# Kernel optimization log

Measured on AMD Instinct MI355X. Metric: run time of the kernel, lower is better.

The kernel has to match this reference:

```python
import jax, jax.numpy as jnp
import numpy as np

B, C, W, H = 4, 256, 64, 64
CQ = C // 8


def setup_inputs() -> dict:
    key = jax.random.key(0)
    ks = jax.random.split(key, 8)
    s = 1.0 / np.sqrt(C)
    return {
        "x": jax.random.normal(ks[0], (B, C, W, H), dtype=jnp.float32),
        "Wq": jax.random.normal(ks[1], (CQ, C), dtype=jnp.float32) * s,
        "bq": jnp.zeros((CQ,), dtype=jnp.float32),
        "Wk": jax.random.normal(ks[2], (CQ, C), dtype=jnp.float32) * s,
        "bk": jnp.zeros((CQ,), dtype=jnp.float32),
        "Wv": jax.random.normal(ks[3], (C, C), dtype=jnp.float32) * s,
        "bv": jnp.zeros((C,), dtype=jnp.float32),
        "gamma": jnp.zeros((1,), dtype=jnp.float32),
    }


def reference(x, Wq, bq, Wk, bk, Wv, bv, gamma):
    b, c, w, h = x.shape
    n = w * h
    xf = x.reshape(b, c, n)  # [B, C, N] flattened spatial
    # 1x1 convs are channel-wise linear maps
    q = jnp.einsum("dc,bcn->bnd", Wq, xf) + bq  # [B, N, C//8]
    k = jnp.einsum("dc,bcn->bdn", Wk, xf) + bk[None, :, None]  # [B, C//8, N]
    v = jnp.einsum("dc,bcn->bdn", Wv, xf) + bv[None, :, None]  # [B, C, N]
    attn = jax.nn.softmax(jnp.einsum("bnd,bdm->bnm", q, k), axis=-1)  # [B, N, N]
    # out[b, c, n] = sum_m v[b, c, m] * attn[b, n, m]
    out = jnp.einsum("bdm,bnm->bdn", v, attn).reshape(b, c, w, h)
    return gamma[0] * out + x
```

## Files before the change

kernel.cpp:

```cpp
#include <hip/hip_runtime.h>
#include <hip/hip_bf16.h>

#define CC 256
#define NN 4096
#define CQ 32
#define LOG2E 1.4426950408889634f

using short4v = __attribute__((ext_vector_type(4))) short;
using short8 = __attribute__((ext_vector_type(8))) short;
using f32x4  = __attribute__((ext_vector_type(4))) float;

static __device__ __forceinline__ short f2bf(float f) {
  __hip_bfloat16 h = __float2bfloat16(f);
  return *reinterpret_cast<short*>(&h);
}

__global__ __launch_bounds__(256) void prep_kernel(
    const float* __restrict__ Wq, const float* __restrict__ Wk,
    const float* __restrict__ Wv, __hip_bfloat16* __restrict__ Wf)
{
  int t = blockIdx.x*256 + threadIdx.x;
  int lane = t & 63, frag = t >> 6;
  int tile = frag >> 3, kc = frag & 7;
  int l15 = lane & 15, quad = lane >> 4;
  int R = tile*16 + l15;
  int k0 = kc*32 + quad*8;
  const float* src;
  if (R < 32)       src = Wq + (size_t)R*CC + k0;
  else if (R < 64)  src = Wk + (size_t)(R-32)*CC + k0;
  else              src = Wv + (size_t)(R-64)*CC + k0;
  float4 a = *(const float4*)(src);
  float4 c = *(const float4*)(src + 4);
  short8 o;
  o[0]=f2bf(a.x); o[1]=f2bf(a.y); o[2]=f2bf(a.z); o[3]=f2bf(a.w);
  o[4]=f2bf(c.x); o[5]=f2bf(c.y); o[6]=f2bf(c.z); o[7]=f2bf(c.w);
  *reinterpret_cast<short8*>(reinterpret_cast<short*>(Wf) + (size_t)t*8) = o;
}

__global__ __launch_bounds__(512, 4) void qkv_kernel(
    const float* __restrict__ x, const __hip_bfloat16* __restrict__ Wf,
    const float* __restrict__ bq, const float* __restrict__ bk,
    const float* __restrict__ bv,
    __hip_bfloat16* __restrict__ qb, __hip_bfloat16* __restrict__ kb,
    __hip_bfloat16* __restrict__ vb)
{
  const int b  = blockIdx.y;
  const int n0 = blockIdx.x * 32;
  const int tid = threadIdx.x;
  const int lane = tid & 63;
  const int w = __builtin_amdgcn_readfirstlane(tid >> 6);
  const int l15 = lane & 15, quad = lane >> 4;

  __shared__ __align__(16) short Xl[16*64*8];
  __shared__ __align__(16) short Vr[8][16][32];

  const float* xb = x + (size_t)b*CC*NN;
#pragma unroll
  for (int i = 0; i < 2; i++) {
    int s = tid + 512*i;
    int g = s >> 6, ln = s & 63;
    int nr = g >> 3, kc = g & 7;
    int l15s = ln & 15, quads = ln >> 4;
    int n = n0 + nr*16 + l15s;
    int c0 = kc*32 + quads*8;
    float v[8];
#pragma unroll
    for (int j = 0; j < 8; j++) v[j] = xb[(size_t)(c0 + j)*NN + n];
    short8 sv;
#pragma unroll
    for (int j = 0; j < 8; j++) sv[j] = f2bf(v[j]);
    *reinterpret_cast<short8*>(&Xl[(size_t)s*8]) = sv;
  }
  __syncthreads();

  const short* wfp = reinterpret_cast<const short*>(Wf);
  short* qb_s = reinterpret_cast<short*>(qb) + (size_t)b*NN*CQ;
  short* kb_s = reinterpret_cast<short*>(kb) + (size_t)b*NN*CQ;
  short* vb_s = reinterpret_cast<short*>(vb) + (size_t)b*CC*NN;

#define QKV_TILE(T) { \
    const int t_ = (T); \
    short8 Af[8]; \
    _Pragma("unroll") \
    for (int kc = 0; kc < 8; kc++) \
      Af[kc] = *(const short8*)(wfp + ((size_t)(t_*8 + kc)*64 + lane)*8); \
    f32x4 ac0 = {0.f,0.f,0.f,0.f}, ac1 = {0.f,0.f,0.f,0.f}; \
    _Pragma("unroll") \
    for (int kc = 0; kc < 8; kc++) { \
      short8 B0 = *(const short8*)(&Xl[((     kc)*64 + lane)*8]); \
      short8 B1 = *(const short8*)(&Xl[((8 +  kc)*64 + lane)*8]); \
      ac0 = __builtin_amdgcn_mfma_f32_16x16x32_bf16(Af[kc], B0, ac0, 0,0,0); \
      ac1 = __builtin_amdgcn_mfma_f32_16x16x32_bf16(Af[kc], B1, ac1, 0,0,0); \
    } \
    if (t_ < 2) { \
      int d0 = t_*16 + quad*4; \
      short4v p0, p1; \
      _Pragma("unroll") \
      for (int r = 0; r < 4; r++) { \
        float bb = bq[d0 + r]; \
        p0[r] = f2bf(LOG2E*(ac0[r] + bb)); \
        p1[r] = f2bf(LOG2E*(ac1[r] + bb)); \
      } \
      *(short4v*)(qb_s + (size_t)(n0      + l15)*CQ + d0) = p0; \
      *(short4v*)(qb_s + (size_t)(n0 + 16 + l15)*CQ + d0) = p1; \
    } else if (t_ < 4) { \
      int d0 = (t_-2)*16 + quad*4; \
      short4v p0, p1; \
      _Pragma("unroll") \
      for (int r = 0; r < 4; r++) { \
        float bb = bk[d0 + r]; \
        p0[r] = f2bf(ac0[r] + bb); \
        p1[r] = f2bf(ac1[r] + bb); \
      } \
      *(short4v*)(kb_s + (size_t)(n0      + l15)*CQ + d0) = p0; \
      *(short4v*)(kb_s + (size_t)(n0 + 16 + l15)*CQ + d0) = p1; \
    } else { \
      int rv0 = (t_-4)*16; \
      _Pragma("unroll") \
      for (int r = 0; r < 4; r++) { \
        float bb = bv[rv0 + quad*4 + r]; \
        Vr[w][quad*4 + r][     l15] = f2bf(ac0[r] + bb); \
        Vr[w][quad*4 + r][16 + l15] = f2bf(ac1[r] + bb); \
      } \
      int row = lane >> 2, cb = (lane & 3)*8; \
      short8 tv = *(const short8*)(&Vr[w][row][cb]); \
      *(short8*)(vb_s + (size_t)(rv0 + row)*NN + n0 + cb) = tv; \
    } }

  QKV_TILE(w);
  QKV_TILE(8 + w);
  if (w < 4) { QKV_TILE(16 + w); }
#undef QKV_TILE
}

__global__ __launch_bounds__(1024, 4) void attn_kernel(
    const __hip_bfloat16* __restrict__ qb, const __hip_bfloat16* __restrict__ kb,
    const __hip_bfloat16* __restrict__ vb,
    const float* __restrict__ x, const float* __restrict__ gamma,
    float* __restrict__ out)
{
  const int Bk = blockIdx.x;
  const int b = (Bk & 7) >> 1;
  const int n0 = ((Bk >> 3)*2 + (Bk & 1)) * 64;
  const int tid = threadIdx.x;
  const int lane = tid & 63;
  const int w = __builtin_amdgcn_readfirstlane(tid >> 6);
  const int sg = w & 3;
  const int mh = (w >> 2) & 1;
  const int ph = w >> 3;
  const int l15 = lane & 15, quad = lane >> 4;
  const int mbase = mh*32 + ph*16;

  __shared__ __align__(16) short Vs[256][76];
  __shared__ __align__(16) short Ps[64][76];
  __shared__ float Lbuf[4][64];

  const short* qbase = (const short*)qb + (size_t)b*NN*CQ;
  const short* kbase = (const short*)kb + (size_t)b*NN*CQ;
  const short* vbase = (const short*)vb + (size_t)b*CC*NN;

  short8 aq = *(const short8*)(qbase + (size_t)(n0 + sg*16 + l15)*CQ + quad*8);

  const int vr = tid >> 2, sh = tid & 3;

  short* pdst = &Ps[sg*16 + l15][mbase + quad*4];

  short8 vfa, vfb, kf;
  vfa = *(const short8*)(vbase + (size_t)vr*NN + sh*16);
  vfb = *(const short8*)(vbase + (size_t)vr*NN + sh*16 + 8);
  kf  = *(const short8*)(kbase + (size_t)(mbase + l15)*CQ + quad*8);
  *(short8*)(&Vs[vr][sh*16    ]) = vfa;
  *(short8*)(&Vs[vr][sh*16 + 8]) = vfb;

  f32x4 acc[4][2];
#pragma unroll
  for (int cg = 0; cg < 4; cg++)
#pragma unroll
    for (int ng = 0; ng < 2; ng++) acc[cg][ng] = (f32x4){0.f,0.f,0.f,0.f};
  float lsum = 0.f;

  __syncthreads();

  for (int T = 0; T < 64; T++) {
    short8 nva, nvb, nk;
    if (T < 63) {
      const short* vp = vbase + (size_t)vr*NN + (T+1)*64 + sh*16;
      nva = *(const short8*)(vp);
      nvb = *(const short8*)(vp + 8);
      nk  = *(const short8*)(kbase + (size_t)((T+1)*64 + mbase + l15)*CQ + quad*8);
    }

    f32x4 z = {0.f,0.f,0.f,0.f};
    f32x4 S = __builtin_amdgcn_mfma_f32_16x16x32_bf16(kf, aq, z, 0,0,0);
    {
      short4v pk;
#pragma unroll
      for (int r = 0; r < 4; r++) {
        float e = __builtin_amdgcn_exp2f(S[r]);
        lsum += e;
        pk[r] = f2bf(e);
      }
      *(short4v*)(pdst) = pk;
    }
    __syncthreads();

    short8 ap0 = *(const short8*)(&Ps[(ph*2    )*16 + l15][mh*32 + quad*8]);
    short8 ap1 = *(const short8*)(&Ps[(ph*2 + 1)*16 + l15][mh*32 + quad*8]);
#pragma unroll
    for (int cg = 0; cg < 4; cg++) {
      short8 av = *(const short8*)(&Vs[sg*64 + cg*16 + l15][mh*32 + quad*8]);
      acc[cg][0] = __builtin_amdgcn_mfma_f32_16x16x32_bf16(av, ap0, acc[cg][0], 0,0,0);
      acc[cg][1] = __builtin_amdgcn_mfma_f32_16x16x32_bf16(av, ap1, acc[cg][1], 0,0,0);
    }
    __syncthreads();

    if (T < 63) {
      *(short8*)(&Vs[vr][sh*16    ]) = nva;
      *(short8*)(&Vs[vr][sh*16 + 8]) = nvb;
      kf = nk;
    }
  }

  {
    float s = lsum;
    s += __shfl_xor(s, 16); s += __shfl_xor(s, 32);
    if (quad == 0) Lbuf[mh*2 + ph][sg*16 + l15] = s;
  }

  float* poolf = reinterpret_cast<float*>(&Vs[0][0]);
  __syncthreads();
#pragma unroll
  for (int g = 0; g < 2; g++) {
    if (mh == 1 && (sg >> 1) == g) {
#pragma unroll
      for (int cg = 0; cg < 4; cg++)
#pragma unroll
        for (int ng = 0; ng < 2; ng++)
#pragma unroll
          for (int r = 0; r < 4; r++)
            poolf[(sg & 1)*4096 + (cg*16 + quad*4 + r)*64 + (ph*2 + ng)*16 + l15] = acc[cg][ng][r];
    }
    __syncthreads();
    if (mh == 0 && (sg >> 1) == g) {
#pragma unroll
      for (int cg = 0; cg < 4; cg++)
#pragma unroll
        for (int ng = 0; ng < 2; ng++)
#pragma unroll
          for (int r = 0; r < 4; r++)
            acc[cg][ng][r] += poolf[(sg & 1)*4096 + (cg*16 + quad*4 + r)*64 + (ph*2 + ng)*16 + l15];
    }
    __syncthreads();
  }

  if (mh == 0) {
    const float gm = gamma[0];
    float Lv[2];
#pragma unroll
    for (int ng = 0; ng < 2; ng++) {
      int n = (ph*2 + ng)*16 + l15;
      Lv[ng] = 1.0f / (Lbuf[0][n] + Lbuf[1][n] + Lbuf[2][n] + Lbuf[3][n]);
    }
#pragma unroll
    for (int cg = 0; cg < 4; cg++) {
#pragma unroll
      for (int ng = 0; ng < 2; ng++) {
#pragma unroll
        for (int r = 0; r < 4; r++) {
          size_t idx = ((size_t)b*CC + sg*64 + cg*16 + quad*4 + r)*NN + n0 + (ph*2 + ng)*16 + l15;
          out[idx] = gm * acc[cg][ng][r] * Lv[ng] + x[idx];
        }
      }
    }
  }
}

extern "C" void kernel_launch(void* const* d_in, const int* in_sizes, int n_in,
                              void* d_out, int out_size, void* d_ws, size_t ws_size,
                              hipStream_t stream) {
  const float* x     = (const float*)d_in[0];
  const float* Wq    = (const float*)d_in[1];
  const float* bq    = (const float*)d_in[2];
  const float* Wk    = (const float*)d_in[3];
  const float* bk    = (const float*)d_in[4];
  const float* Wv    = (const float*)d_in[5];
  const float* bv    = (const float*)d_in[6];
  const float* gamma = (const float*)d_in[7];
  float* out = (float*)d_out;

  char* ws = (char*)d_ws;
  if (ws_size < (11u << 20)) return;
  __hip_bfloat16* qb = (__hip_bfloat16*)(ws);
  __hip_bfloat16* kb = (__hip_bfloat16*)(ws + (1u << 20));
  __hip_bfloat16* vb = (__hip_bfloat16*)(ws + (2u << 20));
  __hip_bfloat16* Wf = (__hip_bfloat16*)(ws + (10u << 20));

  prep_kernel<<<dim3(40), 256, 0, stream>>>(Wq, Wk, Wv, Wf);
  qkv_kernel<<<dim3(128, 4), 512, 0, stream>>>(x, Wf, bq, bk, bv, qb, kb, vb);
  attn_kernel<<<dim3(256), 1024, 0, stream>>>(qb, kb, vb, x, gamma, out);
}
```

Measured before the change: 145.9 us.

## Fuse prep, QKV projection and attention into one cooperative kernel with grid syncs

Replaces three separate kernel launches with one cooperative kernel of 256 blocks that runs weight conversion, QKV projection and attention in sequence, separated by grid-wide syncs. Each block handles the same batch and position tile across phases and shares one static shared-memory buffer. The aim is to remove launch overhead and the gaps between kernels. In exchange it depends on cooperative launch succeeding with all 256 blocks of 1024 threads co-resident, and it adds grid.sync costs. If the cooperative launch fails it falls back to the old three launches.

```diff
diff --git a/kernel.cpp b/kernel.cpp
--- a/kernel.cpp
+++ b/kernel.cpp
@@ -1,5 +1,8 @@
 #include <hip/hip_runtime.h>
 #include <hip/hip_bf16.h>
+#include <hip/hip_cooperative_groups.h>
+
+namespace cg = cooperative_groups;
 
 #define CC 256
 #define NN 4096
@@ -13,6 +16,276 @@
 static __device__ __forceinline__ short f2bf(float f) {
   __hip_bfloat16 h = __float2bfloat16(f);
   return *reinterpret_cast<short*>(&h);
+}
+
+__global__ __launch_bounds__(1024, 4) void fused_kernel(
+    const float* __restrict__ x,
+    const float* __restrict__ Wq, const float* __restrict__ Wk,
+    const float* __restrict__ Wv,
+    const float* __restrict__ bq, const float* __restrict__ bk,
+    const float* __restrict__ bv,
+    const float* __restrict__ gamma,
+    __hip_bfloat16* __restrict__ Wf,
+    __hip_bfloat16* __restrict__ qb, __hip_bfloat16* __restrict__ kb,
+    __hip_bfloat16* __restrict__ vb,
+    float* __restrict__ out)
+{
+  cg::grid_group grid = cg::this_grid();
+  const int Bk = blockIdx.x;
+  const int tid = threadIdx.x;
+
+  __shared__ __align__(16) char smem[49664];
+
+  {
+    int t = Bk*1024 + tid;
+    if (t < 10240) {
+      int lane = t & 63, frag = t >> 6;
+      int tile = frag >> 3, kc = frag & 7;
+      int l15 = lane & 15, quad = lane >> 4;
+      int R = tile*16 + l15;
+      int k0 = kc*32 + quad*8;
+      const float* src;
+      if (R < 32)       src = Wq + (size_t)R*CC + k0;
+      else if (R < 64)  src = Wk + (size_t)(R-32)*CC + k0;
+      else              src = Wv + (size_t)(R-64)*CC + k0;
+      float4 a = *(const float4*)(src);
+      float4 c = *(const float4*)(src + 4);
+      short8 o;
+      o[0]=f2bf(a.x); o[1]=f2bf(a.y); o[2]=f2bf(a.z); o[3]=f2bf(a.w);
+      o[4]=f2bf(c.x); o[5]=f2bf(c.y); o[6]=f2bf(c.z); o[7]=f2bf(c.w);
+      *reinterpret_cast<short8*>(reinterpret_cast<short*>(Wf) + (size_t)t*8) = o;
+    }
+  }
+  grid.sync();
+
+  {
+    const int b    = (Bk & 7) >> 1;
+    const int half = tid >> 9;
+    const int n0   = ((Bk >> 3)*2 + (Bk & 1))*64 + half*32;
+    const int tid_h = tid & 511;
+    const int lane = tid & 63;
+    const int w  = tid_h >> 6;
+    const int w2 = tid >> 6;
+    const int l15 = lane & 15, quad = lane >> 4;
+
+    short* Xl = reinterpret_cast<short*>(smem) + (size_t)half*8192;
+    short* Vr = reinterpret_cast<short*>(smem) + 16384;
+
+    const float* xb = x + (size_t)b*CC*NN;
+#pragma unroll
+    for (int i = 0; i < 2; i++) {
+      int s = tid_h + 512*i;
+      int g = s >> 6, ln = s & 63;
+      int nr = g >> 3, kc = g & 7;
+      int l15s = ln & 15, quads = ln >> 4;
+      int n = n0 + nr*16 + l15s;
+      int c0 = kc*32 + quads*8;
+      float v[8];
+#pragma unroll
+      for (int j = 0; j < 8; j++) v[j] = xb[(size_t)(c0 + j)*NN + n];
+      short8 sv;
+#pragma unroll
+      for (int j = 0; j < 8; j++) sv[j] = f2bf(v[j]);
+      *reinterpret_cast<short8*>(&Xl[(size_t)s*8]) = sv;
+    }
+    __syncthreads();
+
+    const short* wfp = reinterpret_cast<const short*>(Wf);
+    short* qb_s = reinterpret_cast<short*>(qb) + (size_t)b*NN*CQ;
+    short* kb_s = reinterpret_cast<short*>(kb) + (size_t)b*NN*CQ;
+    short* vb_s = reinterpret_cast<short*>(vb) + (size_t)b*CC*NN;
+
+#define QKV_TILE(T) { \
+    const int t_ = (T); \
+    short8 Af[8]; \
+    _Pragma("unroll") \
+    for (int kc = 0; kc < 8; kc++) \
+      Af[kc] = *(const short8*)(wfp + ((size_t)(t_*8 + kc)*64 + lane)*8); \
+    f32x4 ac0 = {0.f,0.f,0.f,0.f}, ac1 = {0.f,0.f,0.f,0.f}; \
+    _Pragma("unroll") \
+    for (int kc = 0; kc < 8; kc++) { \
+      short8 B0 = *(const short8*)(&Xl[((     kc)*64 + lane)*8]); \
+      short8 B1 = *(const short8*)(&Xl[((8 +  kc)*64 + lane)*8]); \
+      ac0 = __builtin_amdgcn_mfma_f32_16x16x32_bf16(Af[kc], B0, ac0, 0,0,0); \
+      ac1 = __builtin_amdgcn_mfma_f32_16x16x32_bf16(Af[kc], B1, ac1, 0,0,0); \
+    } \
+    if (t_ < 2) { \
+      int d0 = t_*16 + quad*4; \
+      short4v p0, p1; \
+      _Pragma("unroll") \
+      for (int r = 0; r < 4; r++) { \
+        float bb = bq[d0 + r]; \
+        p0[r] = f2bf(LOG2E*(ac0[r] + bb)); \
+        p1[r] = f2bf(LOG2E*(ac1[r] + bb)); \
+      } \
+      *(short4v*)(qb_s + (size_t)(n0      + l15)*CQ + d0) = p0; \
+      *(short4v*)(qb_s + (size_t)(n0 + 16 + l15)*CQ + d0) = p1; \
+    } else if (t_ < 4) { \
+      int d0 = (t_-2)*16 + quad*4; \
+      short4v p0, p1; \
+      _Pragma("unroll") \
+      for (int r = 0; r < 4; r++) { \
+        float bb = bk[d0 + r]; \
+        p0[r] = f2bf(ac0[r] + bb); \
+        p1[r] = f2bf(ac1[r] + bb); \
+      } \
+      *(short4v*)(kb_s + (size_t)(n0      + l15)*CQ + d0) = p0; \
+      *(short4v*)(kb_s + (size_t)(n0 + 16 + l15)*CQ + d0) = p1; \
+    } else { \
+      int rv0 = (t_-4)*16; \
+      _Pragma("unroll") \
+      for (int r = 0; r < 4; r++) { \
+        float bb = bv[rv0 + quad*4 + r]; \
+        Vr[(size_t)w2*512 + (quad*4 + r)*32 +      l15] = f2bf(ac0[r] + bb); \
+        Vr[(size_t)w2*512 + (quad*4 + r)*32 + 16 + l15] = f2bf(ac1[r] + bb); \
+      } \
+      int row = lane >> 2, cb = (lane & 3)*8; \
+      short8 tv = *(const short8*)(&Vr[(size_t)w2*512 + row*32 + cb]); \
+      *(short8*)(vb_s + (size_t)(rv0 + row)*NN + n0 + cb) = tv; \
+    } }
+
+    QKV_TILE(w);
+    QKV_TILE(8 + w);
+    if (w < 4) { QKV_TILE(16 + w); }
+#undef QKV_TILE
+  }
+
+  __threadfence();
+  grid.sync();
+
+  {
+    const int b = (Bk & 7) >> 1;
+    const int n0 = ((Bk >> 3)*2 + (Bk & 1)) * 64;
+    const int lane = tid & 63;
+    const int w = __builtin_amdgcn_readfirstlane(tid >> 6);
+    const int sg = w & 3;
+    const int mh = (w >> 2) & 1;
+    const int ph = w >> 3;
+    const int l15 = lane & 15, quad = lane >> 4;
+    const int mbase = mh*32 + ph*16;
+
+    auto Vs   = reinterpret_cast<short (*)[76]>(smem);
+    auto Ps   = reinterpret_cast<short (*)[76]>(smem + 38912);
+    auto Lbuf = reinterpret_cast<float (*)[64]>(smem + 48640);
+
+    const short* qbase = (const short*)qb + (size_t)b*NN*CQ;
+    const short* kbase = (const short*)kb + (size_t)b*NN*CQ;
+    const short* vbase = (const short*)vb + (size_t)b*CC*NN;
+
+    short8 aq = *(const short8*)(qbase + (size_t)(n0 + sg*16 + l15)*CQ + quad*8);
+
+    const int vr = tid >> 2, sh = tid & 3;
+    short* pdst = &Ps[sg*16 + l15][mbase + quad*4];
+
+    short8 vfa, vfb, kf;
+    vfa = *(const short8*)(vbase + (size_t)vr*NN + sh*16);
+    vfb = *(const short8*)(vbase + (size_t)vr*NN + sh*16 + 8);
+    kf  = *(const short8*)(kbase + (size_t)(mbase + l15)*CQ + quad*8);
+    *(short8*)(&Vs[vr][sh*16    ]) = vfa;
+    *(short8*)(&Vs[vr][sh*16 + 8]) = vfb;
+
+    f32x4 acc[4][2];
+#pragma unroll
+    for (int cg2 = 0; cg2 < 4; cg2++)
+#pragma unroll
+      for (int ng = 0; ng < 2; ng++) acc[cg2][ng] = (f32x4){0.f,0.f,0.f,0.f};
+    float lsum = 0.f;
+
+    __syncthreads();
+
+    for (int T = 0; T < 64; T++) {
+      short8 nva, nvb, nk;
+      if (T < 63) {
+        const short* vp = vbase + (size_t)vr*NN + (T+1)*64 + sh*16;
+        nva = *(const short8*)(vp);
+        nvb = *(const short8*)(vp + 8);
+        nk  = *(const short8*)(kbase + (size_t)((T+1)*64 + mbase + l15)*CQ + quad*8);
+      }
+
+      f32x4 z = {0.f,0.f,0.f,0.f};
+      f32x4 S = __builtin_amdgcn_mfma_f32_16x16x32_bf16(kf, aq, z, 0,0,0);
+      {
+        short4v pk;
+#pragma unroll
+        for (int r = 0; r < 4; r++) {
+          float e = __builtin_amdgcn_exp2f(S[r]);
+          lsum += e;
+          pk[r] = f2bf(e);
+        }
+        *(short4v*)(pdst) = pk;
+      }
+      __syncthreads();
+
+      short8 ap0 = *(const short8*)(&Ps[(ph*2    )*16 + l15][mh*32 + quad*8]);
+      short8 ap1 = *(const short8*)(&Ps[(ph*2 + 1)*16 + l15][mh*32 + quad*8]);
+#pragma unroll
+      for (int cg2 = 0; cg2 < 4; cg2++) {
+        short8 av = *(const short8*)(&Vs[sg*64 + cg2*16 + l15][mh*32 + quad*8]);
+        acc[cg2][0] = __builtin_amdgcn_mfma_f32_16x16x32_bf16(av, ap0, acc[cg2][0], 0,0,0);
+        acc[cg2][1] = __builtin_amdgcn_mfma_f32_16x16x32_bf16(av, ap1, acc[cg2][1], 0,0,0);
+      }
+      __syncthreads();
+
+      if (T < 63) {
+        *(short8*)(&Vs[vr][sh*16    ]) = nva;
+        *(short8*)(&Vs[vr][sh*16 + 8]) = nvb;
+        kf = nk;
+      }
+    }
+
+    {
+      float s = lsum;
+      s += __shfl_xor(s, 16); s += __shfl_xor(s, 32);
+      if (quad == 0) Lbuf[mh*2 + ph][sg*16 + l15] = s;
+    }
+
+    float* poolf = reinterpret_cast<float*>(smem);
+    __syncthreads();
+#pragma unroll
+    for (int g = 0; g < 2; g++) {
+      if (mh == 1 && (sg >> 1) == g) {
+#pragma unroll
+        for (int cg2 = 0; cg2 < 4; cg2++)
+#pragma unroll
+          for (int ng = 0; ng < 2; ng++)
+#pragma unroll
+            for (int r = 0; r < 4; r++)
+              poolf[(sg & 1)*4096 + (cg2*16 + quad*4 + r)*64 + (ph*2 + ng)*16 + l15] = acc[cg2][ng][r];
+      }
+      __syncthreads();
+      if (mh == 0 && (sg >> 1) == g) {
+#pragma unroll
+        for (int cg2 = 0; cg2 < 4; cg2++)
+#pragma unroll
+          for (int ng = 0; ng < 2; ng++)
+#pragma unroll
+            for (int r = 0; r < 4; r++)
+              acc[cg2][ng][r] += poolf[(sg & 1)*4096 + (cg2*16 + quad*4 + r)*64 + (ph*2 + ng)*16 + l15];
+      }
+      __syncthreads();
+    }
+
+    if (mh == 0) {
+      const float gm = gamma[0];
+      float Lv[2];
+#pragma unroll
+      for (int ng = 0; ng < 2; ng++) {
+        int n = (ph*2 + ng)*16 + l15;
+        Lv[ng] = 1.0f / (Lbuf[0][n] + Lbuf[1][n] + Lbuf[2][n] + Lbuf[3][n]);
+      }
+#pragma unroll
+      for (int cg2 = 0; cg2 < 4; cg2++) {
+#pragma unroll
+        for (int ng = 0; ng < 2; ng++) {
+#pragma unroll
+          for (int r = 0; r < 4; r++) {
+            size_t idx = ((size_t)b*CC + sg*64 + cg2*16 + quad*4 + r)*NN + n0 + (ph*2 + ng)*16 + l15;
+            out[idx] = gm * acc[cg2][ng][r] * Lv[ng] + x[idx];
+          }
+        }
+      }
+    }
+  }
 }
 
 __global__ __launch_bounds__(256) void prep_kernel(
@@ -162,7 +435,6 @@
   short8 aq = *(const short8*)(qbase + (size_t)(n0 + sg*16 + l15)*CQ + quad*8);
 
   const int vr = tid >> 2, sh = tid & 3;
-
   short* pdst = &Ps[sg*16 + l15][mbase + quad*4];
 
   short8 vfa, vfb, kf;
@@ -295,7 +567,16 @@
   __hip_bfloat16* vb = (__hip_bfloat16*)(ws + (2u << 20));
   __hip_bfloat16* Wf = (__hip_bfloat16*)(ws + (10u << 20));
 
-  prep_kernel<<<dim3(40), 256, 0, stream>>>(Wq, Wk, Wv, Wf);
-  qkv_kernel<<<dim3(128, 4), 512, 0, stream>>>(x, Wf, bq, bk, bv, qb, kb, vb);
-  attn_kernel<<<dim3(256), 1024, 0, stream>>>(qb, kb, vb, x, gamma, out);
+  void* args[] = { (void*)&x, (void*)&Wq, (void*)&Wk, (void*)&Wv,
+                   (void*)&bq, (void*)&bk, (void*)&bv, (void*)&gamma,
+                   (void*)&Wf, (void*)&qb, (void*)&kb, (void*)&vb,
+                   (void*)&out };
+  hipError_t err = hipLaunchCooperativeKernel(
+      (const void*)fused_kernel, dim3(256), dim3(1024), args, 0, stream);
+
+  if (err != hipSuccess) {
+    prep_kernel<<<dim3(40), 256, 0, stream>>>(Wq, Wk, Wv, Wf);
+    qkv_kernel<<<dim3(128, 4), 512, 0, stream>>>(x, Wf, bq, bk, bv, qb, kb, vb);
+    attn_kernel<<<dim3(256), 1024, 0, stream>>>(qb, kb, vb, x, gamma, out);
+  }
 }
```

Result: slower. 490.4 us (+236.1%).
